# Performance work log

Hardware: AMD Instinct MI355X
Metric: run time of the kernel (lower is better)

Reference implementation:

```python
import jax, jax.numpy as jnp
import numpy as np

N_NODES = 100000
N_FEAT = 512
N_HID = 256
N_CLASS = 10
N_EDGES = 3200000


def setup_inputs() -> dict:
    key = jax.random.key(0)
    ks = jax.random.split(key, 8)
    x = jax.random.normal(ks[0], (N_NODES, N_FEAT), dtype=jnp.float32)
    edge_src = jax.random.randint(ks[1], (N_EDGES,), 0, N_NODES, dtype=jnp.int32)
    edge_dst = jax.random.randint(ks[2], (N_EDGES,), 0, N_NODES, dtype=jnp.int32)
    edge_weight = jax.random.uniform(ks[3], (N_EDGES,), dtype=jnp.float32)
    # Glorot-style init like the torch GraphConvolution reset_parameters
    s1 = 1.0 / np.sqrt(N_HID)
    s2 = 1.0 / np.sqrt(N_CLASS)
    W1 = jax.random.uniform(ks[4], (N_FEAT, N_HID), dtype=jnp.float32, minval=-s1, maxval=s1)
    b1 = jax.random.uniform(ks[5], (N_HID,), dtype=jnp.float32, minval=-s1, maxval=s1)
    W2 = jax.random.uniform(ks[6], (N_HID, N_CLASS), dtype=jnp.float32, minval=-s2, maxval=s2)
    b2 = jax.random.uniform(ks[7], (N_CLASS,), dtype=jnp.float32, minval=-s2, maxval=s2)
    return {"x": x, "edge_src": edge_src, "edge_dst": edge_dst,
            "edge_weight": edge_weight, "W1": W1, "b1": b1, "W2": W2, "b2": b2}


def reference(x, edge_src, edge_dst, edge_weight, W1, b1, W2, b2):
    n = x.shape[0]

    def gcn_layer(h, W, b):
        # dense transform: [N, d_in] @ [d_in, d_out]
        support = h @ W
        # sparse aggregation: out[dst] += w * support[src]  (spmm(adj, support))
        msgs = support[edge_src] * edge_weight[:, None]
        agg = jax.ops.segment_sum(msgs, edge_dst, num_segments=n)
        return agg + b

    h = jax.nn.relu(gcn_layer(x, W1, b1))
    # dropout is identity in eval mode
    logits = gcn_layer(h, W2, b2)
    return jax.nn.log_softmax(logits, axis=1)
```

## Files before the change

### kernel.cpp

```cpp
#include <hip/hip_runtime.h>
#include <hip/hip_bf16.h>
#include <math.h>

#define NFEAT 512
#define NHID 256
#define NCLASS 10
#define BCAP 20000

typedef unsigned short u16;
typedef unsigned char u8;
using frag_ab = __attribute__((ext_vector_type(8))) short;
using frag_cd = __attribute__((ext_vector_type(4))) float;
using f32x2 = __attribute__((ext_vector_type(2))) float;

__device__ inline u16 f2bf(float f) {
    __hip_bfloat16 b = __float2bfloat16(f);
    return __builtin_bit_cast(unsigned short, b);
}
__device__ inline float bf2f(u16 u) {
    unsigned int t = ((unsigned int)u) << 16;
    return __builtin_bit_cast(float, t);
}
__device__ inline float i2f(int i) { return __builtin_bit_cast(float, i); }
__device__ inline u8 f2fp8(float v) {
    int p = __builtin_amdgcn_cvt_pk_fp8_f32(v, v, 0, false);
    return (u8)(p & 0xff);
}


__global__ void k_binit(int* bcur, int nb) {
    int tid = threadIdx.x;
    if (tid < nb) bcur[tid] = tid * BCAP;
}

__global__ void k_bin(const int* __restrict__ src, const int* __restrict__ dst,
                      const float* __restrict__ w, int* __restrict__ bcur,
                      int2* __restrict__ sstag, int E) {
    __shared__ int hist[256];
    __shared__ int gbase[256];
    int tid = threadIdx.x;
    int e0 = blockIdx.x * 4096;
    hist[tid] = 0;
    __syncthreads();
#pragma unroll
    for (int i = 0; i < 16; i++) {
        int e = e0 + i * 256 + tid;
        if (e < E) atomicAdd(&hist[dst[e] >> 9], 1);
    }
    __syncthreads();
    int cnt = hist[tid];
    if (cnt > 0) gbase[tid] = atomicAdd(&bcur[tid], cnt);
    hist[tid] = 0;
    __syncthreads();
#pragma unroll
    for (int i = 0; i < 16; i++) {
        int e = e0 + i * 256 + tid;
        if (e < E) {
            int d = dst[e];
            int b = d >> 9;
            int l = atomicAdd(&hist[b], 1);
            int2 q;
            q.x = src[e];
            q.y = (__builtin_bit_cast(int, w[e]) & ~511) | (d & 511);
            sstag[gbase[b] + l] = q;
        }
    }
}

__global__ void k_bscan(const int* __restrict__ bcur, int* __restrict__ bbase, int nb) {
    __shared__ int tmp[256];
    int tid = threadIdx.x;
    int cnt = (tid < nb) ? (bcur[tid] - tid * BCAP) : 0;
    tmp[tid] = cnt;
    __syncthreads();
    for (int off = 1; off < 256; off <<= 1) {
        int t = (tid >= off) ? tmp[tid - off] : 0;
        __syncthreads();
        tmp[tid] += t;
        __syncthreads();
    }
    if (tid < nb) bbase[tid] = tmp[tid] - cnt;
    if (tid == nb - 1) bbase[nb] = tmp[tid];
}

__global__ __launch_bounds__(1024)
void k_build(const int2* __restrict__ sstag, const int* __restrict__ bcur,
             const int* __restrict__ bbase, int* __restrict__ rowptr,
             int2* __restrict__ eg, int N) {
    __shared__ int hist[512];
    __shared__ int scn[512];
    __shared__ int lcur[512];
    int b = blockIdx.x;
    int tid = threadIdx.x;
    int base = bbase[b];
    int cnt = bcur[b] - b * BCAP;
    const int2* ss = sstag + (size_t)b * BCAP;
    if (tid < 512) hist[tid] = 0;
    __syncthreads();
    for (int i = tid; i < cnt; i += 1024) atomicAdd(&hist[ss[i].y & 511], 1);
    __syncthreads();
    if (tid < 512) scn[tid] = hist[tid];
    __syncthreads();
    for (int off = 1; off < 512; off <<= 1) {
        int v = (tid < 512 && tid >= off) ? scn[tid - off] : 0;
        __syncthreads();
        if (tid < 512) scn[tid] += v;
        __syncthreads();
    }
    if (tid < 512) {
        int ex = scn[tid] - hist[tid];
        lcur[tid] = ex;
        int d = b * 512 + tid;
        if (d <= N) rowptr[d] = base + ex;
    }
    __syncthreads();
    for (int i = tid; i < cnt; i += 1024) {
        int2 q = ss[i];
        int dl = q.y & 511;
        q.y &= ~511;
        int p = atomicAdd(&lcur[dl], 1);
        eg[base + p] = q;
    }
}


__global__ void k_w1t(const float* __restrict__ W1, u16* __restrict__ W1T) {
    int i = blockIdx.x * 256 + threadIdx.x;
    int k = i / NHID, n = i % NHID;
    W1T[n * NFEAT + k] = f2bf(W1[i]);
}

#define BROW_STRIDE_B 80
__global__ __launch_bounds__(256, 2)
void k_gemm1(const float* __restrict__ x, const u16* __restrict__ W1T,
             u8* __restrict__ sup1, int N) {
    __shared__ char lB[256 * BROW_STRIDE_B];
    int tid = threadIdx.x;
    int wid = tid >> 6, lane = tid & 63;
    int lrow = lane & 15, kq = lane >> 4;
    long rowbase = (long)blockIdx.x * 128;

    long r0 = rowbase + wid * 32 + lrow;
    long r1 = r0 + 16;
    long ra0 = (r0 < N) ? r0 : (long)(N - 1);
    long ra1 = (r1 < N) ? r1 : (long)(N - 1);
    const float* xr0 = x + ra0 * NFEAT;
    const float* xr1 = x + ra1 * NFEAT;

    frag_cd acc[2][16];
#pragma unroll
    for (int t = 0; t < 2; t++)
#pragma unroll
        for (int nt = 0; nt < 16; nt++) acc[t][nt] = (frag_cd){0.f, 0.f, 0.f, 0.f};

    for (int k0 = 0; k0 < NFEAT; k0 += 32) {
        __syncthreads();
#pragma unroll
        for (int j = 0; j < 4; j++) {
            int id = j * 256 + tid;
            int n = id >> 2, q = id & 3;
            int4 v = *(const int4*)(W1T + n * NFEAT + k0 + q * 8);
            *(int4*)(lB + n * BROW_STRIDE_B + q * 16) = v;
        }
        __syncthreads();

        int ko = k0 + kq * 8;
        float4 a00 = *(const float4*)(xr0 + ko);
        float4 a01 = *(const float4*)(xr0 + ko + 4);
        float4 a10 = *(const float4*)(xr1 + ko);
        float4 a11 = *(const float4*)(xr1 + ko + 4);
        frag_ab af0, af1;
        af0[0] = (short)f2bf(a00.x); af0[1] = (short)f2bf(a00.y);
        af0[2] = (short)f2bf(a00.z); af0[3] = (short)f2bf(a00.w);
        af0[4] = (short)f2bf(a01.x); af0[5] = (short)f2bf(a01.y);
        af0[6] = (short)f2bf(a01.z); af0[7] = (short)f2bf(a01.w);
        af1[0] = (short)f2bf(a10.x); af1[1] = (short)f2bf(a10.y);
        af1[2] = (short)f2bf(a10.z); af1[3] = (short)f2bf(a10.w);
        af1[4] = (short)f2bf(a11.x); af1[5] = (short)f2bf(a11.y);
        af1[6] = (short)f2bf(a11.z); af1[7] = (short)f2bf(a11.w);

        const char* lbase = lB + lrow * BROW_STRIDE_B + kq * 16;
#pragma unroll
        for (int nt = 0; nt < 16; nt++) {
            frag_ab bfr = *(const frag_ab*)(lbase + nt * 16 * BROW_STRIDE_B);
            acc[0][nt] = __builtin_amdgcn_mfma_f32_16x16x32_bf16(af0, bfr, acc[0][nt], 0, 0, 0);
            acc[1][nt] = __builtin_amdgcn_mfma_f32_16x16x32_bf16(af1, bfr, acc[1][nt], 0, 0, 0);
        }
    }

#pragma unroll
    for (int t = 0; t < 2; t++) {
#pragma unroll
        for (int nt = 0; nt < 16; nt++) {
#pragma unroll
            for (int r = 0; r < 4; r++) {
                long grow = rowbase + wid * 32 + t * 16 + kq * 4 + r;
                if (grow < N)
                    sup1[grow * NHID + nt * 16 + lrow] = f2fp8(acc[t][nt][r]);
            }
        }
    }
}

__global__ void k_agg1(const u8* __restrict__ sup1, const int* __restrict__ rowptr,
                       const int2* __restrict__ eg, const float* __restrict__ b1,
                       u16* __restrict__ h, int N) {
    int wid = threadIdx.x >> 6, lane = threadIdx.x & 63;
    int node = blockIdx.x * 4 + wid;
    if (node >= N) return;
    int rp0 = rowptr[node], rp1 = rowptr[node + 1];
    float a0 = 0.f, a1 = 0.f, a2 = 0.f, a3 = 0.f;
    int e = rp0;
    for (; e + 4 <= rp1; e += 4) {
        int2 q0 = eg[e], q1 = eg[e + 1], q2 = eg[e + 2], q3 = eg[e + 3];
        int v0 = *(const int*)(sup1 + (long)q0.x * NHID + lane * 4);
        int v1 = *(const int*)(sup1 + (long)q1.x * NHID + lane * 4);
        int v2 = *(const int*)(sup1 + (long)q2.x * NHID + lane * 4);
        int v3 = *(const int*)(sup1 + (long)q3.x * NHID + lane * 4);
        float w0 = i2f(q0.y), w1 = i2f(q1.y), w2 = i2f(q2.y), w3 = i2f(q3.y);
        f32x2 l0 = __builtin_amdgcn_cvt_pk_f32_fp8(v0, false);
        f32x2 h0 = __builtin_amdgcn_cvt_pk_f32_fp8(v0, true);
        f32x2 l1 = __builtin_amdgcn_cvt_pk_f32_fp8(v1, false);
        f32x2 h1 = __builtin_amdgcn_cvt_pk_f32_fp8(v1, true);
        f32x2 l2 = __builtin_amdgcn_cvt_pk_f32_fp8(v2, false);
        f32x2 h2 = __builtin_amdgcn_cvt_pk_f32_fp8(v2, true);
        f32x2 l3 = __builtin_amdgcn_cvt_pk_f32_fp8(v3, false);
        f32x2 h3 = __builtin_amdgcn_cvt_pk_f32_fp8(v3, true);
        a0 += w0 * l0[0]; a1 += w0 * l0[1]; a2 += w0 * h0[0]; a3 += w0 * h0[1];
        a0 += w1 * l1[0]; a1 += w1 * l1[1]; a2 += w1 * h1[0]; a3 += w1 * h1[1];
        a0 += w2 * l2[0]; a1 += w2 * l2[1]; a2 += w2 * h2[0]; a3 += w2 * h2[1];
        a0 += w3 * l3[0]; a1 += w3 * l3[1]; a2 += w3 * h3[0]; a3 += w3 * h3[1];
    }
    for (; e < rp1; e++) {
        int2 q0 = eg[e];
        float w0 = i2f(q0.y);
        int v0 = *(const int*)(sup1 + (long)q0.x * NHID + lane * 4);
        f32x2 l0 = __builtin_amdgcn_cvt_pk_f32_fp8(v0, false);
        f32x2 h0 = __builtin_amdgcn_cvt_pk_f32_fp8(v0, true);
        a0 += w0 * l0[0]; a1 += w0 * l0[1]; a2 += w0 * h0[0]; a3 += w0 * h0[1];
    }
    float4 bb = *(const float4*)(b1 + lane * 4);
    ushort4 o;
    o.x = f2bf(fmaxf(a0 + bb.x, 0.f));
    o.y = f2bf(fmaxf(a1 + bb.y, 0.f));
    o.z = f2bf(fmaxf(a2 + bb.z, 0.f));
    o.w = f2bf(fmaxf(a3 + bb.w, 0.f));
    *(ushort4*)(h + (long)node * NHID + lane * 4) = o;
}

__global__ void k_gemm2(const u16* __restrict__ h, const float* __restrict__ W2,
                        float* __restrict__ sup2, int N) {
    __shared__ u16 lh[64 * 258];
    __shared__ float lw2[NHID * NCLASS];
    int tid = threadIdx.x;
    int g0 = blockIdx.x * 64;
    for (int i = tid; i < NHID * NCLASS; i += 256) lw2[i] = W2[i];
    for (int g = tid; g < 64 * 64; g += 256) {
        int nl = g >> 6, k4 = (g & 63) << 2;
        int gn = g0 + nl;
        ushort4 v;
        v.x = v.y = v.z = v.w = 0;
        if (gn < N) v = *(const ushort4*)(h + (long)gn * NHID + k4);
        int o = nl * 258 + k4;
        lh[o] = v.x; lh[o + 1] = v.y; lh[o + 2] = v.z; lh[o + 3] = v.w;
    }
    __syncthreads();
    for (int t = tid; t < 64 * NCLASS; t += 256) {
        int nl = t / NCLASS, c = t % NCLASS;
        int gn = g0 + nl;
        const u16* hr = lh + nl * 258;
        float s = 0.f;
#pragma unroll 4
        for (int k = 0; k < NHID; k++) s += bf2f(hr[k]) * lw2[k * NCLASS + c];
        if (gn < N) sup2[(long)gn * NCLASS + c] = s;
    }
}

__global__ void k_out(const float* __restrict__ sup2, const int* __restrict__ rowptr,
                      const int2* __restrict__ eg, const float* __restrict__ b2,
                      float* __restrict__ out, int N) {
    int wid = threadIdx.x >> 6, lane = threadIdx.x & 63;
    int node = blockIdx.x * 4 + wid;
    if (node >= N) return;
    int rp0 = rowptr[node], rp1 = rowptr[node + 1];
    float acc[NCLASS];
#pragma unroll
    for (int c = 0; c < NCLASS; c++) acc[c] = 0.f;
    for (int e = rp0 + lane; e < rp1; e += 64) {
        int2 q = eg[e];
        float w = i2f(q.y);
        const float* sr = sup2 + (long)q.x * NCLASS;
#pragma unroll
        for (int c = 0; c < NCLASS; c++) acc[c] += w * sr[c];
    }
#pragma unroll
    for (int c = 0; c < NCLASS; c++) {
#pragma unroll
        for (int m = 1; m < 64; m <<= 1) acc[c] += __shfl_xor(acc[c], m, 64);
    }
    float logit[NCLASS], mx = -1e30f;
#pragma unroll
    for (int c = 0; c < NCLASS; c++) { logit[c] = acc[c] + b2[c]; mx = fmaxf(mx, logit[c]); }
    float se = 0.f;
#pragma unroll
    for (int c = 0; c < NCLASS; c++) se += expf(logit[c] - mx);
    float lse = mx + logf(se);
    if (lane < NCLASS) {
        float v = 0.f;
#pragma unroll
        for (int c = 0; c < NCLASS; c++) if (lane == c) v = logit[c] - lse;
        out[(long)node * NCLASS + lane] = v;
    }
}


extern "C" void kernel_launch(void* const* d_in, const int* in_sizes, int n_in,
                              void* d_out, int out_size, void* d_ws, size_t ws_size,
                              hipStream_t stream) {
    const float* x   = (const float*)d_in[0];
    const int* esrc0 = (const int*)d_in[1];
    const int* edst0 = (const int*)d_in[2];
    const float* ew0 = (const float*)d_in[3];
    const float* W1  = (const float*)d_in[4];
    const float* b1  = (const float*)d_in[5];
    const float* W2  = (const float*)d_in[6];
    const float* b2  = (const float*)d_in[7];
    float* out = (float*)d_out;

    const int N = in_sizes[0] / NFEAT;
    const int E = in_sizes[1];
    const int NB = (N + 511) >> 9;

    char* ws = (char*)d_ws;
    size_t off = 0;
    auto alloc = [&](size_t bytes) -> void* {
        off = (off + 255) & ~(size_t)255;
        void* p = ws + off;
        off += bytes;
        return p;
    };
    u8*   sup1   = (u8*)alloc((size_t)N * NHID);
    u16*  h      = (u16*)alloc((size_t)N * NHID * 2);
    float* sup2  = (float*)alloc((size_t)N * NCLASS * 4);
    u16*  W1T    = (u16*)alloc((size_t)NFEAT * NHID * 2);
    int*  rowptr = (int*)alloc((size_t)(N + 1) * 4);
    int2* eg     = (int2*)alloc((size_t)E * 8);
    int2* sstag  = (int2*)alloc((size_t)NB * BCAP * 8);
    int*  bcur   = (int*)alloc((size_t)NB * 4);
    int*  bbase  = (int*)alloc((size_t)(NB + 1) * 4);

    k_binit<<<1, 256, 0, stream>>>(bcur, NB);
    k_bin<<<(E + 4095) / 4096, 256, 0, stream>>>(esrc0, edst0, ew0, bcur, sstag, E);
    k_bscan<<<1, 256, 0, stream>>>(bcur, bbase, NB);
    k_build<<<NB, 1024, 0, stream>>>(sstag, bcur, bbase, rowptr, eg, N);
    k_w1t<<<(NFEAT * NHID) / 256, 256, 0, stream>>>(W1, W1T);
    k_gemm1<<<(N + 127) / 128, 256, 0, stream>>>(x, W1T, sup1, N);
    k_agg1<<<(N + 3) / 4, 256, 0, stream>>>(sup1, rowptr, eg, b1, h, N);
    k_gemm2<<<(N + 63) / 64, 256, 0, stream>>>(h, W2, sup2, N);
    k_out<<<(N + 3) / 4, 256, 0, stream>>>(sup2, rowptr, eg, b2, out, N);
}
```

Before: 720.2 us.

## Split agg1 feature columns across blocks and parallelize k_out per class lane

k_agg1 now splits each node's 256-byte fp8 feature row into 8 column slices handled by separate blocks. Within a wave, 8 lanes cover a 32-byte slice while 8 edge groups run in parallel, and partial sums are combined with cross-lane shuffles. sup2 is padded to 16 floats per node so k_out can give each lane one class and gather 4 edges at a time, replacing per-lane 10-element row loads and 60 shuffles. This trades more blocks and redundant rowptr/edge-list reads for better memory-level parallelism and more coalesced gathers.

Result: slower. 997.4 us (+38.5%).

```diff
diff --git a/kernel.cpp b/kernel.cpp
--- a/kernel.cpp
+++ b/kernel.cpp
@@ -205,51 +205,70 @@
 __global__ void k_agg1(const u8* __restrict__ sup1, const int* __restrict__ rowptr,
                        const int2* __restrict__ eg, const float* __restrict__ b1,
                        u16* __restrict__ h, int N) {
+    int slice = blockIdx.x & 7;
+    int nb = blockIdx.x >> 3;
     int wid = threadIdx.x >> 6, lane = threadIdx.x & 63;
-    int node = blockIdx.x * 4 + wid;
+    int node = nb * 4 + wid;
     if (node >= N) return;
+    int esub = lane >> 3;
+    int word = lane & 7;
+    int sofs = slice * 32 + word * 4;
     int rp0 = rowptr[node], rp1 = rowptr[node + 1];
     float a0 = 0.f, a1 = 0.f, a2 = 0.f, a3 = 0.f;
+
     int e = rp0;
-    for (; e + 4 <= rp1; e += 4) {
-        int2 q0 = eg[e], q1 = eg[e + 1], q2 = eg[e + 2], q3 = eg[e + 3];
-        int v0 = *(const int*)(sup1 + (long)q0.x * NHID + lane * 4);
-        int v1 = *(const int*)(sup1 + (long)q1.x * NHID + lane * 4);
-        int v2 = *(const int*)(sup1 + (long)q2.x * NHID + lane * 4);
-        int v3 = *(const int*)(sup1 + (long)q3.x * NHID + lane * 4);
-        float w0 = i2f(q0.y), w1 = i2f(q1.y), w2 = i2f(q2.y), w3 = i2f(q3.y);
-        f32x2 l0 = __builtin_amdgcn_cvt_pk_f32_fp8(v0, false);
-        f32x2 h0 = __builtin_amdgcn_cvt_pk_f32_fp8(v0, true);
-        f32x2 l1 = __builtin_amdgcn_cvt_pk_f32_fp8(v1, false);
-        f32x2 h1 = __builtin_amdgcn_cvt_pk_f32_fp8(v1, true);
-        f32x2 l2 = __builtin_amdgcn_cvt_pk_f32_fp8(v2, false);
-        f32x2 h2 = __builtin_amdgcn_cvt_pk_f32_fp8(v2, true);
-        f32x2 l3 = __builtin_amdgcn_cvt_pk_f32_fp8(v3, false);
-        f32x2 h3 = __builtin_amdgcn_cvt_pk_f32_fp8(v3, true);
-        a0 += w0 * l0[0]; a1 += w0 * l0[1]; a2 += w0 * h0[0]; a3 += w0 * h0[1];
-        a0 += w1 * l1[0]; a1 += w1 * l1[1]; a2 += w1 * h1[0]; a3 += w1 * h1[1];
-        a0 += w2 * l2[0]; a1 += w2 * l2[1]; a2 += w2 * h2[0]; a3 += w2 * h2[1];
-        a0 += w3 * l3[0]; a1 += w3 * l3[1]; a2 += w3 * h3[0]; a3 += w3 * h3[1];
-    }
-    for (; e < rp1; e++) {
-        int2 q0 = eg[e];
-        float w0 = i2f(q0.y);
-        int v0 = *(const int*)(sup1 + (long)q0.x * NHID + lane * 4);
-        f32x2 l0 = __builtin_amdgcn_cvt_pk_f32_fp8(v0, false);
-        f32x2 h0 = __builtin_amdgcn_cvt_pk_f32_fp8(v0, true);
-        a0 += w0 * l0[0]; a1 += w0 * l0[1]; a2 += w0 * h0[0]; a3 += w0 * h0[1];
-    }
-    float4 bb = *(const float4*)(b1 + lane * 4);
-    ushort4 o;
-    o.x = f2bf(fmaxf(a0 + bb.x, 0.f));
-    o.y = f2bf(fmaxf(a1 + bb.y, 0.f));
-    o.z = f2bf(fmaxf(a2 + bb.z, 0.f));
-    o.w = f2bf(fmaxf(a3 + bb.w, 0.f));
-    *(ushort4*)(h + (long)node * NHID + lane * 4) = o;
+    for (; e + 16 <= rp1; e += 16) {
+        int2 qA = eg[e + esub];
+        int2 qB = eg[e + 8 + esub];
+        int vA = *(const int*)(sup1 + (long)qA.x * NHID + sofs);
+        int vB = *(const int*)(sup1 + (long)qB.x * NHID + sofs);
+        float wA = i2f(qA.y), wB = i2f(qB.y);
+        f32x2 lA = __builtin_amdgcn_cvt_pk_f32_fp8(vA, false);
+        f32x2 hA = __builtin_amdgcn_cvt_pk_f32_fp8(vA, true);
+        f32x2 lB = __builtin_amdgcn_cvt_pk_f32_fp8(vB, false);
+        f32x2 hB = __builtin_amdgcn_cvt_pk_f32_fp8(vB, true);
+        a0 += wA * lA[0]; a1 += wA * lA[1]; a2 += wA * hA[0]; a3 += wA * hA[1];
+        a0 += wB * lB[0]; a1 += wB * lB[1]; a2 += wB * hB[0]; a3 += wB * hB[1];
+    }
+    for (; e + 8 <= rp1; e += 8) {
+        int2 q = eg[e + esub];
+        int v = *(const int*)(sup1 + (long)q.x * NHID + sofs);
+        float wf = i2f(q.y);
+        f32x2 lo = __builtin_amdgcn_cvt_pk_f32_fp8(v, false);
+        f32x2 hi = __builtin_amdgcn_cvt_pk_f32_fp8(v, true);
+        a0 += wf * lo[0]; a1 += wf * lo[1]; a2 += wf * hi[0]; a3 += wf * hi[1];
+    }
+    if (e < rp1) {
+        int ei = e + esub;
+        if (ei < rp1) {
+            int2 q = eg[ei];
+            int v = *(const int*)(sup1 + (long)q.x * NHID + sofs);
+            float wf = i2f(q.y);
+            f32x2 lo = __builtin_amdgcn_cvt_pk_f32_fp8(v, false);
+            f32x2 hi = __builtin_amdgcn_cvt_pk_f32_fp8(v, true);
+            a0 += wf * lo[0]; a1 += wf * lo[1]; a2 += wf * hi[0]; a3 += wf * hi[1];
+        }
+    }
+#pragma unroll
+    for (int m = 8; m < 64; m <<= 1) {
+        a0 += __shfl_xor(a0, m, 64);
+        a1 += __shfl_xor(a1, m, 64);
+        a2 += __shfl_xor(a2, m, 64);
+        a3 += __shfl_xor(a3, m, 64);
+    }
+    if (esub == 0) {
+        float4 bb = *(const float4*)(b1 + sofs);
+        ushort4 o;
+        o.x = f2bf(fmaxf(a0 + bb.x, 0.f));
+        o.y = f2bf(fmaxf(a1 + bb.y, 0.f));
+        o.z = f2bf(fmaxf(a2 + bb.z, 0.f));
+        o.w = f2bf(fmaxf(a3 + bb.w, 0.f));
+        *(ushort4*)(h + (long)node * NHID + sofs) = o;
+    }
 }
 
 __global__ void k_gemm2(const u16* __restrict__ h, const float* __restrict__ W2,
-                        float* __restrict__ sup2, int N) {
+                        float* __restrict__ sup2p, int N) {
     __shared__ u16 lh[64 * 258];
     __shared__ float lw2[NHID * NCLASS];
     int tid = threadIdx.x;
@@ -265,52 +284,63 @@
         lh[o] = v.x; lh[o + 1] = v.y; lh[o + 2] = v.z; lh[o + 3] = v.w;
     }
     __syncthreads();
-    for (int t = tid; t < 64 * NCLASS; t += 256) {
-        int nl = t / NCLASS, c = t % NCLASS;
+    for (int t = tid; t < 64 * 16; t += 256) {
+        int nl = t >> 4, c = t & 15;
         int gn = g0 + nl;
-        const u16* hr = lh + nl * 258;
         float s = 0.f;
+        if (c < NCLASS) {
+            const u16* hr = lh + nl * 258;
 #pragma unroll 4
-        for (int k = 0; k < NHID; k++) s += bf2f(hr[k]) * lw2[k * NCLASS + c];
-        if (gn < N) sup2[(long)gn * NCLASS + c] = s;
-    }
-}
-
-__global__ void k_out(const float* __restrict__ sup2, const int* __restrict__ rowptr,
+            for (int k = 0; k < NHID; k++) s += bf2f(hr[k]) * lw2[k * NCLASS + c];
+        }
+        if (gn < N) sup2p[(long)gn * 16 + c] = s;
+    }
+}
+
+__global__ void k_out(const float* __restrict__ sup2p, const int* __restrict__ rowptr,
                       const int2* __restrict__ eg, const float* __restrict__ b2,
                       float* __restrict__ out, int N) {
     int wid = threadIdx.x >> 6, lane = threadIdx.x & 63;
     int node = blockIdx.x * 4 + wid;
     if (node >= N) return;
+    int esub = lane >> 4;
+    int c = lane & 15;
     int rp0 = rowptr[node], rp1 = rowptr[node + 1];
-    float acc[NCLASS];
-#pragma unroll
-    for (int c = 0; c < NCLASS; c++) acc[c] = 0.f;
-    for (int e = rp0 + lane; e < rp1; e += 64) {
-        int2 q = eg[e];
-        float w = i2f(q.y);
-        const float* sr = sup2 + (long)q.x * NCLASS;
-#pragma unroll
-        for (int c = 0; c < NCLASS; c++) acc[c] += w * sr[c];
-    }
-#pragma unroll
-    for (int c = 0; c < NCLASS; c++) {
-#pragma unroll
-        for (int m = 1; m < 64; m <<= 1) acc[c] += __shfl_xor(acc[c], m, 64);
-    }
-    float logit[NCLASS], mx = -1e30f;
-#pragma unroll
-    for (int c = 0; c < NCLASS; c++) { logit[c] = acc[c] + b2[c]; mx = fmaxf(mx, logit[c]); }
-    float se = 0.f;
-#pragma unroll
-    for (int c = 0; c < NCLASS; c++) se += expf(logit[c] - mx);
+    float acc = 0.f;
+
+    int e = rp0;
+    for (; e + 8 <= rp1; e += 8) {
+        int2 qA = eg[e + esub];
+        int2 qB = eg[e + 4 + esub];
+        float vA = sup2p[(long)qA.x * 16 + c];
+        float vB = sup2p[(long)qB.x * 16 + c];
+        acc += i2f(qA.y) * vA;
+        acc += i2f(qB.y) * vB;
+    }
+    for (; e + 4 <= rp1; e += 4) {
+        int2 q = eg[e + esub];
+        acc += i2f(q.y) * sup2p[(long)q.x * 16 + c];
+    }
+    if (e < rp1) {
+        int ei = e + esub;
+        if (ei < rp1) {
+            int2 q = eg[ei];
+            acc += i2f(q.y) * sup2p[(long)q.x * 16 + c];
+        }
+    }
+    acc += __shfl_xor(acc, 16, 64);
+    acc += __shfl_xor(acc, 32, 64);
+    float lg = (c < NCLASS) ? (acc + b2[c]) : -1e30f;
+    float mx = lg;
+#pragma unroll
+    for (int m = 1; m < 16; m <<= 1) mx = fmaxf(mx, __shfl_xor(mx, m, 64));
+    float ex = (c < NCLASS) ? expf(lg - mx) : 0.f;
+    float se = ex;
+#pragma unroll
+    for (int m = 1; m < 16; m <<= 1) se += __shfl_xor(se, m, 64);
     float lse = mx + logf(se);
-    if (lane < NCLASS) {
-        float v = 0.f;
-#pragma unroll
-        for (int c = 0; c < NCLASS; c++) if (lane == c) v = logit[c] - lse;
-        out[(long)node * NCLASS + lane] = v;
-    }
+    if (esub == 0 && c < NCLASS)
+        out[(long)node * NCLASS + c] = lg - lse;
 }
 
 
@@ -341,7 +371,7 @@
     };
     u8*   sup1   = (u8*)alloc((size_t)N * NHID);
     u16*  h      = (u16*)alloc((size_t)N * NHID * 2);
-    float* sup2  = (float*)alloc((size_t)N * NCLASS * 4);
+    float* sup2p = (float*)alloc((size_t)N * 16 * 4);
     u16*  W1T    = (u16*)alloc((size_t)NFEAT * NHID * 2);
     int*  rowptr = (int*)alloc((size_t)(N + 1) * 4);
     int2* eg     = (int2*)alloc((size_t)E * 8);
@@ -355,7 +385,7 @@
     k_build<<<NB, 1024, 0, stream>>>(sstag, bcur, bbase, rowptr, eg, N);
     k_w1t<<<(NFEAT * NHID) / 256, 256, 0, stream>>>(W1, W1T);
     k_gemm1<<<(N + 127) / 128, 256, 0, stream>>>(x, W1T, sup1, N);
-    k_agg1<<<(N + 3) / 4, 256, 0, stream>>>(sup1, rowptr, eg, b1, h, N);
-    k_gemm2<<<(N + 63) / 64, 256, 0, stream>>>(h, W2, sup2, N);
-    k_out<<<(N + 3) / 4, 256, 0, stream>>>(sup2, rowptr, eg, b2, out, N);
-}
+    k_agg1<<<((N + 3) / 4) * 8, 256, 0, stream>>>(sup1, rowptr, eg, b1, h, N);
+    k_gemm2<<<(N + 63) / 64, 256, 0, stream>>>(h, W2, sup2p, N);
+    k_out<<<(N + 3) / 4, 256, 0, stream>>>(sup2p, rowptr, eg, b2, out, N);
+}
```
